# Kernel optimization log

Hardware: AMD Instinct MI355X
Metric: run time of the kernel (lower is better)

The kernel has to match this reference:

```python
import jax, jax.numpy as jnp
import numpy as np

N_NODES = 100000
N_EDGES = 1600000
IN_FEATS = 256
N_HEADS = 4
OUT_FEATS = 32
NEG_SLOPE = 0.2


def setup_inputs() -> dict:
    key = jax.random.key(0)
    k0, k1, k2, k3, k4, k5 = jax.random.split(key, 6)
    feat = jax.random.normal(k0, (N_NODES, IN_FEATS), dtype=jnp.float32)
    src = jax.random.randint(k1, (N_EDGES,), 0, N_NODES, dtype=jnp.int32)
    dst = jax.random.randint(k2, (N_EDGES,), 0, N_NODES, dtype=jnp.int32)
    # fc.weight: [num_heads*out_feats, in_feats] (torch Linear layout)
    W = jax.random.normal(k3, (N_HEADS * OUT_FEATS, IN_FEATS), dtype=jnp.float32) * 0.05
    attn_l = jax.random.normal(k4, (1, N_HEADS, OUT_FEATS), dtype=jnp.float32) * 0.1
    attn_r = jax.random.normal(k5, (1, N_HEADS, OUT_FEATS), dtype=jnp.float32) * 0.1
    return {"feat": feat, "src": src, "dst": dst, "W": W, "attn_l": attn_l, "attn_r": attn_r}


def reference(feat, src, dst, W, attn_l, attn_r):
    N = feat.shape[0]
    H, D = attn_l.shape[1], attn_l.shape[2]
    # fc projection -> [N, H, D]
    feat_src = (feat @ W.T).reshape(N, H, D)
    el = jnp.sum(feat_src * attn_l, axis=-1)  # [N, H]
    er = jnp.sum(feat_src * attn_r, axis=-1)  # [N, H]
    # per-edge scores: u_add_v then LeakyReLU  -> [E, H]
    e = jax.nn.leaky_relu(el[src] + er[dst], negative_slope=NEG_SLOPE)
    # edge_softmax: segmented softmax over edges grouped by destination node
    emax = jax.ops.segment_max(e, dst, num_segments=N)  # [N, H]
    emax = jnp.where(jnp.isfinite(emax), emax, jnp.zeros_like(emax))
    ee = jnp.exp(e - emax[dst])  # [E, H]
    denom = jax.ops.segment_sum(ee, dst, num_segments=N)  # [N, H]
    a = ee / denom[dst]  # [E, H]
    # u_mul_e + sum aggregation -> [N, H, D]
    m = feat_src[src] * a[:, :, None]  # [E, H, D]
    rst = jax.ops.segment_sum(m, dst, num_segments=N)
    return rst
```

## Files before the change

### kernel.cpp

```cpp
#include <hip/hip_runtime.h>
#include <hip/hip_bf16.h>
#include <math.h>

#define NN 100000
#define NE 1600000
#define INF_ 256
#define NH 4
#define DH 32
#define NHD 128
#define NEG_SLOPE 0.2f

#define NBC 391
#define STRIDEC 4608
#define EPBC 4096
#define NBLK_BIN 391
#define GEMM_BLKS 782
#define FMAX 1408
#define SMEM_BYTES 37504

typedef __attribute__((ext_vector_type(8))) short bf16x8;
typedef __attribute__((ext_vector_type(4))) float f32x4;

__device__ __forceinline__ unsigned short f2bf(float f) {
    __hip_bfloat16 b = __float2bfloat16(f);
    return *reinterpret_cast<unsigned short*>(&b);
}

__global__ __launch_bounds__(256) void k_prep0(const float* __restrict__ W,
                                               unsigned short* __restrict__ Wimg,
                                               int* __restrict__ gcur) {
    int t = threadIdx.x;
    int b = blockIdx.x;
    if (b == 16) {
        for (int i = t; i < NBC; i += 256) gcur[i] = 0;
        return;
    }
    int i = b * 256 + t;
    int kt = i >> 9;
    int r = (i >> 2) & 127;
    int g = i & 3;
    int slot = g ^ (r & 7);
    const float* s = &W[(size_t)r * INF_ + kt * 32 + g * 8];
    unsigned short tmp[8];
#pragma unroll
    for (int j = 0; j < 8; j++) tmp[j] = f2bf(s[j]);
    *(bf16x8*)&Wimg[(size_t)kt * 8192 + r * 64 + slot * 8] = *(const bf16x8*)tmp;
}

__global__ __launch_bounds__(256) void k_gemmbin(const float* __restrict__ feat,
                                                 const unsigned short* __restrict__ Wimg,
                                                 const int* __restrict__ src,
                                                 const int* __restrict__ dst,
                                                 const float* __restrict__ al,
                                                 const float* __restrict__ ar,
                                                 unsigned short* __restrict__ fsb,
                                                 float* __restrict__ el,
                                                 float* __restrict__ er,
                                                 int* __restrict__ gcur,
                                                 unsigned* __restrict__ packed) {
    __shared__ __align__(16) char smem[SMEM_BYTES];
    const int t = threadIdx.x;

    if (blockIdx.x >= GEMM_BLKS) {
        int hb = blockIdx.x - GEMM_BLKS;
        unsigned* lrec = (unsigned*)smem;
        int* lgpos = (int*)(smem + 16384);
        int* lc   = (int*)(smem + 32768);
        int* wb   = lc + NBC;
        int* loff = wb + NBC;
        int* wsum = loff + NBC;
        for (int i = t; i < NBC; i += 256) lc[i] = 0;
        __syncthreads();
        int base = hb * EPBC;
#pragma unroll 4
        for (int j = 0; j < 16; j++) {
            int e = base + j * 256 + t;
            if (e < NE) atomicAdd(&lc[dst[e] >> 8], 1);
        }
        __syncthreads();
        int i0 = t * 2;
        int c0 = (i0 < NBC) ? lc[i0] : 0;
        int c1 = (i0 + 1 < NBC) ? lc[i0 + 1] : 0;
        int s2 = c0 + c1;
        int lane = t & 63, w = t >> 6;
        int x = s2;
#pragma unroll
        for (int o = 1; o < 64; o <<= 1) {
            int y = __shfl_up(x, o);
            if (lane >= o) x += y;
        }
        if (lane == 63) wsum[w] = x;
        __syncthreads();
        int add = 0;
        for (int j = 0; j < w; j++) add += wsum[j];
        int ex = add + x - s2;
        if (i0 < NBC) loff[i0] = ex;
        if (i0 + 1 < NBC) loff[i0 + 1] = ex + c0;
        for (int i = t; i < NBC; i += 256) {
            int c = lc[i];
            wb[i] = c ? i * STRIDEC + atomicAdd(&gcur[i], c) : 0;
        }
        __syncthreads();
        for (int i = t; i < NBC; i += 256) lc[i] = loff[i];
        __syncthreads();
#pragma unroll 4
        for (int j = 0; j < 16; j++) {
            int e = base + j * 256 + t;
            if (e < NE) {
                int d = dst[e];
                int bk = d >> 8;
                int pos = atomicAdd(&lc[bk], 1);
                lrec[pos] = ((unsigned)src[e] << 8) | (unsigned)(d & 255);
                int g = wb[bk] + (pos - loff[bk]);
                lgpos[pos] = (g < (bk + 1) * STRIDEC) ? g : -1;
            }
        }
        __syncthreads();
        int nedge = NE - base;
        if (nedge > EPBC) nedge = EPBC;
        for (int i = t; i < nedge; i += 256) {
            int g = lgpos[i];
            if (g >= 0) packed[g] = lrec[i];
        }
        return;
    }

    short* sA = (short*)smem;
    short* sB = (short*)(smem + 16384);
    const int brow = blockIdx.x * 128;
    const int wid = t >> 6, lane = t & 63;
    const int wr = wid >> 1, wc = wid & 1;
    const int lg = lane >> 4;
    const int lr = lane & 15;

    f32x4 acc[4][4];
#pragma unroll
    for (int m = 0; m < 4; m++)
#pragma unroll
        for (int n = 0; n < 4; n++) acc[m][n] = (f32x4){0.f, 0.f, 0.f, 0.f};

    const int srow = t >> 1;
    const int cb = (t & 1) * 16;
    const int g0 = cb >> 3;
    const int p0 = (g0 ^ (srow & 7));
    const int p1 = ((g0 + 1) ^ (srow & 7));
    const int grow = brow + srow;
    const bool arow_ok = (grow < NN);
    const char* bimg = (const char*)Wimg;

    float fv[16];
    uint4 wv0, wv1, wv2, wv3;
    if (arow_ok) {
        const float4* pa = (const float4*)&feat[(size_t)grow * INF_ + cb];
        *(float4*)&fv[0] = pa[0];
        *(float4*)&fv[4] = pa[1];
        *(float4*)&fv[8] = pa[2];
        *(float4*)&fv[12] = pa[3];
    } else {
#pragma unroll
        for (int j = 0; j < 16; j++) fv[j] = 0.f;
    }
    wv0 = *(const uint4*)(bimg + t * 16);
    wv1 = *(const uint4*)(bimg + 4096 + t * 16);
    wv2 = *(const uint4*)(bimg + 8192 + t * 16);
    wv3 = *(const uint4*)(bimg + 12288 + t * 16);

    for (int kt = 0; kt < 8; kt++) {
        {
            short sv[16];
#pragma unroll
            for (int j = 0; j < 16; j++) sv[j] = (short)f2bf(fv[j]);
            *(bf16x8*)&sA[srow * 64 + p0 * 8] = *(const bf16x8*)&sv[0];
            *(bf16x8*)&sA[srow * 64 + p1 * 8] = *(const bf16x8*)&sv[8];
            char* bd = (char*)sB;
            *(uint4*)(bd + t * 16) = wv0;
            *(uint4*)(bd + 4096 + t * 16) = wv1;
            *(uint4*)(bd + 8192 + t * 16) = wv2;
            *(uint4*)(bd + 12288 + t * 16) = wv3;
        }
        __syncthreads();
        if (kt < 7) {
            int k0 = (kt + 1) * 32;
            if (arow_ok) {
                const float4* pa = (const float4*)&feat[(size_t)grow * INF_ + k0 + cb];
                *(float4*)&fv[0] = pa[0];
                *(float4*)&fv[4] = pa[1];
                *(float4*)&fv[8] = pa[2];
                *(float4*)&fv[12] = pa[3];
            }
            const char* bsrc = bimg + (size_t)(kt + 1) * 16384;
            wv0 = *(const uint4*)(bsrc + t * 16);
            wv1 = *(const uint4*)(bsrc + 4096 + t * 16);
            wv2 = *(const uint4*)(bsrc + 8192 + t * 16);
            wv3 = *(const uint4*)(bsrc + 12288 + t * 16);
        }
        bf16x8 aF[4], bF[4];
#pragma unroll
        for (int m = 0; m < 4; m++) {
            int r = wr * 64 + m * 16 + lr;
            aF[m] = *(const bf16x8*)&sA[r * 64 + ((lg ^ (r & 7)) * 8)];
        }
#pragma unroll
        for (int n = 0; n < 4; n++) {
            int r = wc * 64 + n * 16 + lr;
            bF[n] = *(const bf16x8*)&sB[r * 64 + ((lg ^ (r & 7)) * 8)];
        }
#pragma unroll
        for (int m = 0; m < 4; m++)
#pragma unroll
            for (int n = 0; n < 4; n++)
                acc[m][n] = __builtin_amdgcn_mfma_f32_16x16x32_bf16(aF[m], bF[n], acc[m][n], 0, 0, 0);
        __syncthreads();
    }
#pragma unroll
    for (int m = 0; m < 4; m++) {
#pragma unroll
        for (int n = 0; n < 4; n++) {
#pragma unroll
            for (int r = 0; r < 4; r++) {
                int gr = brow + wr * 64 + m * 16 + lg * 4 + r;
                if (gr < NN)
                    fsb[(size_t)gr * NHD + wc * 64 + n * 16 + lr] = f2bf(acc[m][n][r]);
            }
        }
    }
    const int hA = wc * 2, hB = wc * 2 + 1;
    const float alA0 = al[hA * 32 + lr], alA1 = al[hA * 32 + 16 + lr];
    const float alB0 = al[hB * 32 + lr], alB1 = al[hB * 32 + 16 + lr];
    const float arA0 = ar[hA * 32 + lr], arA1 = ar[hA * 32 + 16 + lr];
    const float arB0 = ar[hB * 32 + lr], arB1 = ar[hB * 32 + 16 + lr];
#pragma unroll
    for (int m = 0; m < 4; m++) {
#pragma unroll
        for (int r = 0; r < 4; r++) {
            float eA = acc[m][0][r] * alA0 + acc[m][1][r] * alA1;
            float eB = acc[m][2][r] * alB0 + acc[m][3][r] * alB1;
            float fA = acc[m][0][r] * arA0 + acc[m][1][r] * arA1;
            float fB = acc[m][2][r] * arB0 + acc[m][3][r] * arB1;
#pragma unroll
            for (int off = 1; off < 16; off <<= 1) {
                eA += __shfl_xor(eA, off);
                eB += __shfl_xor(eB, off);
                fA += __shfl_xor(fA, off);
                fB += __shfl_xor(fB, off);
            }
            if (lr == 0) {
                int gr = brow + wr * 64 + m * 16 + lg * 4 + r;
                if (gr < NN) {
                    el[gr * 4 + hA] = eA;
                    el[gr * 4 + hB] = eB;
                    er[gr * 4 + hA] = fA;
                    er[gr * 4 + hB] = fB;
                }
            }
        }
    }
}

__global__ __launch_bounds__(256) void k_sortagg(const int* __restrict__ gcur,
                                                 const unsigned* __restrict__ packed,
                                                 const float* __restrict__ el,
                                                 const float* __restrict__ er,
                                                 const uint4* __restrict__ fsb128,
                                                 float* __restrict__ out) {
    __shared__ int lh[64];
    __shared__ int off[65];
    __shared__ int cur[64];
    __shared__ int esrc_l[FMAX];
    int bq = blockIdx.x;
    int b = bq >> 2, quarter = bq & 3;
    int t = threadIdx.x;
    int beg = b * STRIDEC;
    int cnt = gcur[b];
    if (cnt > STRIDEC) cnt = STRIDEC;

    if (t < 64) lh[t] = 0;
    __syncthreads();
    for (int k = t; k < cnt; k += 256) {
        unsigned p = packed[beg + k];
        if (((p >> 6) & 3u) == (unsigned)quarter) atomicAdd(&lh[p & 63u], 1);
    }
    __syncthreads();
    if (t < 64) {
        int v = lh[t];
        int x = v;
#pragma unroll
        for (int o = 1; o < 64; o <<= 1) {
            int y = __shfl_up(x, o);
            if (t >= o) x += y;
        }
        off[t] = x - v;
        cur[t] = x - v;
        if (t == 63) off[64] = x;
    }
    __syncthreads();
    for (int k = t; k < cnt; k += 256) {
        unsigned p = packed[beg + k];
        if (((p >> 6) & 3u) == (unsigned)quarter) {
            int pos = atomicAdd(&cur[p & 63u], 1);
            if (pos < FMAX) esrc_l[pos] = (int)(p >> 8);
        }
    }
    __syncthreads();

    int lane = t & 63;
    int wv = t >> 6;
    int q = lane >> 4;
    int sl = lane & 15;
    int h = sl >> 2;

#define STEP(eV, vV)                                           \
    {                                                          \
        float sc_ = (eV) + rr;                                 \
        sc_ = sc_ > 0.f ? sc_ : NEG_SLOPE * sc_;               \
        float ee = __expf(sc_);                                \
        den += ee;                                             \
        a0 += ee * __uint_as_float((vV).x << 16);              \
        a1 += ee * __uint_as_float((vV).x & 0xFFFF0000u);      \
        a2 += ee * __uint_as_float((vV).y << 16);              \
        a3 += ee * __uint_as_float((vV).y & 0xFFFF0000u);      \
        a4 += ee * __uint_as_float((vV).z << 16);              \
        a5 += ee * __uint_as_float((vV).z & 0xFFFF0000u);      \
        a6 += ee * __uint_as_float((vV).w << 16);              \
        a7 += ee * __uint_as_float((vV).w & 0xFFFF0000u);      \
    }

    for (int ln = wv * 16; ln < wv * 16 + 16; ln++) {
        int node = (b << 8) + (quarter << 6) + ln;
        if (node >= NN) break;
        int bg = off[ln];
        int en = off[ln + 1];
        if (en > FMAX) en = FMAX;
        float rr = er[node * 4 + h];
        float den = 0.f;
        float a0 = 0.f, a1 = 0.f, a2 = 0.f, a3 = 0.f;
        float a4 = 0.f, a5 = 0.f, a6 = 0.f, a7 = 0.f;
        int k = bg + q;
        for (; k + 4 < en; k += 8) {
            int s0 = esrc_l[k];
            int s1 = esrc_l[k + 4];
            uint4 v0 = fsb128[(size_t)s0 * 16 + sl];
            uint4 v1 = fsb128[(size_t)s1 * 16 + sl];
            float e0 = el[s0 * 4 + h];
            float e1 = el[s1 * 4 + h];
            STEP(e0, v0)
            STEP(e1, v1)
        }
        for (; k < en; k += 4) {
            int s = esrc_l[k];
            uint4 vv = fsb128[(size_t)s * 16 + sl];
            float eV = el[s * 4 + h];
            STEP(eV, vv)
        }
#pragma unroll
        for (int o = 16; o <= 32; o <<= 1) {
            a0 += __shfl_xor(a0, o);
            a1 += __shfl_xor(a1, o);
            a2 += __shfl_xor(a2, o);
            a3 += __shfl_xor(a3, o);
            a4 += __shfl_xor(a4, o);
            a5 += __shfl_xor(a5, o);
            a6 += __shfl_xor(a6, o);
            a7 += __shfl_xor(a7, o);
            den += __shfl_xor(den, o);
        }
        if (q == 0) {
            float inv = den > 0.f ? 1.0f / den : 0.f;
            float4 o0, o1;
            o0.x = a0 * inv; o0.y = a1 * inv; o0.z = a2 * inv; o0.w = a3 * inv;
            o1.x = a4 * inv; o1.y = a5 * inv; o1.z = a6 * inv; o1.w = a7 * inv;
            float* p = &out[(size_t)node * NHD + sl * 8];
            *(float4*)p = o0;
            *(float4*)(p + 4) = o1;
        }
    }
#undef STEP
}

extern "C" void kernel_launch(void* const* d_in, const int* in_sizes, int n_in,
                              void* d_out, int out_size, void* d_ws, size_t ws_size,
                              hipStream_t stream) {
    const float* feat = (const float*)d_in[0];
    const int* src = (const int*)d_in[1];
    const int* dst = (const int*)d_in[2];
    const float* W = (const float*)d_in[3];
    const float* al = (const float*)d_in[4];
    const float* ar = (const float*)d_in[5];
    float* out = (float*)d_out;

    char* ws = (char*)d_ws;
    unsigned short* fsb = (unsigned short*)ws;   ws += (size_t)NN * NHD * 2;
    unsigned* packed = (unsigned*)ws;            ws += (size_t)NBC * STRIDEC * 4;
    float* el = (float*)ws;                      ws += (size_t)NN * NH * 4;
    float* er = (float*)ws;                      ws += (size_t)NN * NH * 4;
    int* gcur = (int*)ws;                        ws += (size_t)NBC * 4;
    unsigned short* Wimg = (unsigned short*)ws;  ws += (size_t)8 * 8192 * 2;

    k_prep0<<<17, 256, 0, stream>>>(W, Wimg, gcur);
    k_gemmbin<<<GEMM_BLKS + NBLK_BIN, 256, 0, stream>>>(feat, Wimg, src, dst,
                                                        al, ar, fsb, el, er,
                                                        gcur, packed);
    k_sortagg<<<NBC * 4, 256, 0, stream>>>(gcur, packed, el, er,
                                           (const uint4*)fsb, out);
}
```

Baseline: 146.2 us.

## Assign one destination node per 16-lane group and split buckets into eighths

The aggregation kernel now splits each 256-node bucket into eighths instead of quarters, launching twice as many blocks with a smaller shared edge list. Each 16-lane group handles a whole destination node on its own, so the cross-group shuffle reduction goes away and the edge loop is unrolled by four to keep more gathers in flight. The cost is that each block rescans the full bucket's packed edge list, doubling that redundant read traffic, and load balance now depends on per-node degree variance within a group.

```diff
diff --git a/kernel.cpp b/kernel.cpp
--- a/kernel.cpp
+++ b/kernel.cpp
@@ -15,7 +15,7 @@
 #define EPBC 4096
 #define NBLK_BIN 391
 #define GEMM_BLKS 782
-#define FMAX 1408
+#define FMAX 768
 #define SMEM_BYTES 37504
 
 typedef __attribute__((ext_vector_type(8))) short bf16x8;
@@ -263,41 +263,41 @@
                                                  const float* __restrict__ er,
                                                  const uint4* __restrict__ fsb128,
                                                  float* __restrict__ out) {
-    __shared__ int lh[64];
-    __shared__ int off[65];
-    __shared__ int cur[64];
+    __shared__ int lh[32];
+    __shared__ int off[33];
+    __shared__ int cur[32];
     __shared__ int esrc_l[FMAX];
     int bq = blockIdx.x;
-    int b = bq >> 2, quarter = bq & 3;
+    int b = bq >> 3, eighth = bq & 7;
     int t = threadIdx.x;
     int beg = b * STRIDEC;
     int cnt = gcur[b];
     if (cnt > STRIDEC) cnt = STRIDEC;
 
-    if (t < 64) lh[t] = 0;
+    if (t < 32) lh[t] = 0;
     __syncthreads();
     for (int k = t; k < cnt; k += 256) {
         unsigned p = packed[beg + k];
-        if (((p >> 6) & 3u) == (unsigned)quarter) atomicAdd(&lh[p & 63u], 1);
+        if (((p >> 5) & 7u) == (unsigned)eighth) atomicAdd(&lh[p & 31u], 1);
     }
     __syncthreads();
-    if (t < 64) {
+    if (t < 32) {
         int v = lh[t];
         int x = v;
 #pragma unroll
-        for (int o = 1; o < 64; o <<= 1) {
+        for (int o = 1; o < 32; o <<= 1) {
             int y = __shfl_up(x, o);
             if (t >= o) x += y;
         }
         off[t] = x - v;
         cur[t] = x - v;
-        if (t == 63) off[64] = x;
+        if (t == 31) off[32] = x;
     }
     __syncthreads();
     for (int k = t; k < cnt; k += 256) {
         unsigned p = packed[beg + k];
-        if (((p >> 6) & 3u) == (unsigned)quarter) {
-            int pos = atomicAdd(&cur[p & 63u], 1);
+        if (((p >> 5) & 7u) == (unsigned)eighth) {
+            int pos = atomicAdd(&cur[p & 31u], 1);
             if (pos < FMAX) esrc_l[pos] = (int)(p >> 8);
         }
     }
@@ -305,7 +305,7 @@
 
     int lane = t & 63;
     int wv = t >> 6;
-    int q = lane >> 4;
+    int g = lane >> 4;
     int sl = lane & 15;
     int h = sl >> 2;
 
@@ -325,46 +325,44 @@
         a7 += ee * __uint_as_float((vV).w & 0xFFFF0000u);      \
     }
 
-    for (int ln = wv * 16; ln < wv * 16 + 16; ln++) {
-        int node = (b << 8) + (quarter << 6) + ln;
-        if (node >= NN) break;
-        int bg = off[ln];
-        int en = off[ln + 1];
+#pragma unroll
+    for (int r = 0; r < 2; r++) {
+        int ln = wv * 8 + r * 4 + g;
+        int node = (b << 8) + (eighth << 5) + ln;
+        bool ok = (node < NN);
+        int bg = ok ? off[ln] : 0;
+        int en = ok ? off[ln + 1] : 0;
         if (en > FMAX) en = FMAX;
-        float rr = er[node * 4 + h];
+        float rr = ok ? er[node * 4 + h] : 0.f;
         float den = 0.f;
         float a0 = 0.f, a1 = 0.f, a2 = 0.f, a3 = 0.f;
         float a4 = 0.f, a5 = 0.f, a6 = 0.f, a7 = 0.f;
-        int k = bg + q;
-        for (; k + 4 < en; k += 8) {
+        int k = bg;
+        for (; k + 3 < en; k += 4) {
             int s0 = esrc_l[k];
-            int s1 = esrc_l[k + 4];
+            int s1 = esrc_l[k + 1];
+            int s2 = esrc_l[k + 2];
+            int s3 = esrc_l[k + 3];
             uint4 v0 = fsb128[(size_t)s0 * 16 + sl];
             uint4 v1 = fsb128[(size_t)s1 * 16 + sl];
+            uint4 v2 = fsb128[(size_t)s2 * 16 + sl];
+            uint4 v3 = fsb128[(size_t)s3 * 16 + sl];
             float e0 = el[s0 * 4 + h];
             float e1 = el[s1 * 4 + h];
+            float e2 = el[s2 * 4 + h];
+            float e3 = el[s3 * 4 + h];
             STEP(e0, v0)
             STEP(e1, v1)
-        }
-        for (; k < en; k += 4) {
+            STEP(e2, v2)
+            STEP(e3, v3)
+        }
+        for (; k < en; k++) {
             int s = esrc_l[k];
             uint4 vv = fsb128[(size_t)s * 16 + sl];
             float eV = el[s * 4 + h];
             STEP(eV, vv)
         }
-#pragma unroll
-        for (int o = 16; o <= 32; o <<= 1) {
-            a0 += __shfl_xor(a0, o);
-            a1 += __shfl_xor(a1, o);
-            a2 += __shfl_xor(a2, o);
-            a3 += __shfl_xor(a3, o);
-            a4 += __shfl_xor(a4, o);
-            a5 += __shfl_xor(a5, o);
-            a6 += __shfl_xor(a6, o);
-            a7 += __shfl_xor(a7, o);
-            den += __shfl_xor(den, o);
-        }
-        if (q == 0) {
+        if (ok) {
             float inv = den > 0.f ? 1.0f / den : 0.f;
             float4 o0, o1;
             o0.x = a0 * inv; o0.y = a1 * inv; o0.z = a2 * inv; o0.w = a3 * inv;
@@ -400,6 +398,6 @@
     k_gemmbin<<<GEMM_BLKS + NBLK_BIN, 256, 0, stream>>>(feat, Wimg, src, dst,
                                                         al, ar, fsb, el, er,
                                                         gcur, packed);
-    k_sortagg<<<NBC * 4, 256, 0, stream>>>(gcur, packed, el, er,
+    k_sortagg<<<NBC * 8, 256, 0, stream>>>(gcur, packed, el, er,
                                            (const uint4*)fsb, out);
 }
```

New measurement: 150.3 us. 2.8% more time.

## Split sort and aggregation into separate kernels with one wavefront per node

Applied to the files above, without the earlier changes.

The fused sort+aggregate kernel becomes two kernels. The first does a full per-bucket counting sort of packed edges into a global CSR-like esrc array plus per-node offset/count metadata. The second assigns one 64-lane wavefront per destination node. The binning blocks now come first in the grid and store a 16-bit bucket id instead of a precomputed global position, which shrinks shared memory. This targets load imbalance and the quadruple rescanning of packed edges, at the cost of an extra launch and an esrc global write and read.

```diff
diff --git a/kernel.cpp b/kernel.cpp
--- a/kernel.cpp
+++ b/kernel.cpp
@@ -15,8 +15,7 @@
 #define EPBC 4096
 #define NBLK_BIN 391
 #define GEMM_BLKS 782
-#define FMAX 1408
-#define SMEM_BYTES 37504
+#define SMEM_BYTES 32768
 
 typedef __attribute__((ext_vector_type(8))) short bf16x8;
 typedef __attribute__((ext_vector_type(4))) float f32x4;
@@ -61,11 +60,11 @@
     __shared__ __align__(16) char smem[SMEM_BYTES];
     const int t = threadIdx.x;
 
-    if (blockIdx.x >= GEMM_BLKS) {
-        int hb = blockIdx.x - GEMM_BLKS;
+    if (blockIdx.x < NBLK_BIN) {
+        int hb = blockIdx.x;
         unsigned* lrec = (unsigned*)smem;
-        int* lgpos = (int*)(smem + 16384);
-        int* lc   = (int*)(smem + 32768);
+        unsigned short* lbk = (unsigned short*)(smem + 16384);
+        int* lc   = (int*)(smem + 24576);
         int* wb   = lc + NBC;
         int* loff = wb + NBC;
         int* wsum = loff + NBC;
@@ -111,23 +110,24 @@
                 int bk = d >> 8;
                 int pos = atomicAdd(&lc[bk], 1);
                 lrec[pos] = ((unsigned)src[e] << 8) | (unsigned)(d & 255);
-                int g = wb[bk] + (pos - loff[bk]);
-                lgpos[pos] = (g < (bk + 1) * STRIDEC) ? g : -1;
+                lbk[pos] = (unsigned short)bk;
             }
         }
         __syncthreads();
         int nedge = NE - base;
         if (nedge > EPBC) nedge = EPBC;
         for (int i = t; i < nedge; i += 256) {
-            int g = lgpos[i];
-            if (g >= 0) packed[g] = lrec[i];
+            int bk = lbk[i];
+            int g = wb[bk] + (i - loff[bk]);
+            if (g < (bk + 1) * STRIDEC)
+                packed[g] = lrec[i];
         }
         return;
     }
 
     short* sA = (short*)smem;
     short* sB = (short*)(smem + 16384);
-    const int brow = blockIdx.x * 128;
+    const int brow = (blockIdx.x - NBLK_BIN) * 128;
     const int wid = t >> 6, lane = t & 63;
     const int wr = wid >> 1, wc = wid & 1;
     const int lg = lane >> 4;
@@ -257,57 +257,72 @@
     }
 }
 
-__global__ __launch_bounds__(256) void k_sortagg(const int* __restrict__ gcur,
-                                                 const unsigned* __restrict__ packed,
-                                                 const float* __restrict__ el,
-                                                 const float* __restrict__ er,
-                                                 const uint4* __restrict__ fsb128,
-                                                 float* __restrict__ out) {
-    __shared__ int lh[64];
-    __shared__ int off[65];
-    __shared__ int cur[64];
-    __shared__ int esrc_l[FMAX];
-    int bq = blockIdx.x;
-    int b = bq >> 2, quarter = bq & 3;
-    int t = threadIdx.x;
+__global__ __launch_bounds__(256) void k_sort(const int* __restrict__ gcur,
+                                              const unsigned* __restrict__ packed,
+                                              int* __restrict__ esrc,
+                                              int2* __restrict__ rowmeta) {
+    __shared__ int lh[256];
+    __shared__ int off[256];
+    __shared__ int cur[256];
+    __shared__ int wsum[4];
+    __shared__ int es[STRIDEC];
+    int b = blockIdx.x, t = threadIdx.x;
     int beg = b * STRIDEC;
     int cnt = gcur[b];
     if (cnt > STRIDEC) cnt = STRIDEC;
 
-    if (t < 64) lh[t] = 0;
+    lh[t] = 0;
+    __syncthreads();
+    for (int k = t; k < cnt; k += 256)
+        atomicAdd(&lh[packed[beg + k] & 255u], 1);
+    __syncthreads();
+    int v = lh[t];
+    int lane = t & 63, w = t >> 6;
+    int x = v;
+#pragma unroll
+    for (int o = 1; o < 64; o <<= 1) {
+        int y = __shfl_up(x, o);
+        if (lane >= o) x += y;
+    }
+    if (lane == 63) wsum[w] = x;
+    __syncthreads();
+    int add = 0;
+    for (int j = 0; j < w; j++) add += wsum[j];
+    int excl = add + x - v;
+    off[t] = excl;
+    cur[t] = excl;
+    int node = (b << 8) + t;
+    if (node < NN) rowmeta[node] = make_int2(beg + excl, v);
     __syncthreads();
     for (int k = t; k < cnt; k += 256) {
         unsigned p = packed[beg + k];
-        if (((p >> 6) & 3u) == (unsigned)quarter) atomicAdd(&lh[p & 63u], 1);
+        int pos = atomicAdd(&cur[p & 255u], 1);
+        es[pos] = (int)(p >> 8);
     }
     __syncthreads();
-    if (t < 64) {
-        int v = lh[t];
-        int x = v;
-#pragma unroll
-        for (int o = 1; o < 64; o <<= 1) {
-            int y = __shfl_up(x, o);
-            if (t >= o) x += y;
-        }
-        off[t] = x - v;
-        cur[t] = x - v;
-        if (t == 63) off[64] = x;
-    }
-    __syncthreads();
-    for (int k = t; k < cnt; k += 256) {
-        unsigned p = packed[beg + k];
-        if (((p >> 6) & 3u) == (unsigned)quarter) {
-            int pos = atomicAdd(&cur[p & 63u], 1);
-            if (pos < FMAX) esrc_l[pos] = (int)(p >> 8);
-        }
-    }
-    __syncthreads();
-
-    int lane = t & 63;
-    int wv = t >> 6;
+    for (int k = t; k < cnt; k += 256) esrc[beg + k] = es[k];
+}
+
+__global__ __launch_bounds__(256) void k_agg(const int2* __restrict__ rowmeta,
+                                             const int* __restrict__ esrc,
+                                             const float* __restrict__ el,
+                                             const float* __restrict__ er,
+                                             const uint4* __restrict__ fsb128,
+                                             float* __restrict__ out) {
+    int gid = blockIdx.x * blockDim.x + threadIdx.x;
+    int node = gid >> 6;
+    int lane = gid & 63;
+    if (node >= NN) return;
     int q = lane >> 4;
     int sl = lane & 15;
     int h = sl >> 2;
+    int2 md = rowmeta[node];
+    int beg = md.x;
+    int end = md.x + md.y;
+    float rr = er[node * 4 + h];
+    float den = 0.f;
+    float a0 = 0.f, a1 = 0.f, a2 = 0.f, a3 = 0.f;
+    float a4 = 0.f, a5 = 0.f, a6 = 0.f, a7 = 0.f;
 
 #define STEP(eV, vV)                                           \
     {                                                          \
@@ -325,56 +340,47 @@
         a7 += ee * __uint_as_float((vV).w & 0xFFFF0000u);      \
     }
 
-    for (int ln = wv * 16; ln < wv * 16 + 16; ln++) {
-        int node = (b << 8) + (quarter << 6) + ln;
-        if (node >= NN) break;
-        int bg = off[ln];
-        int en = off[ln + 1];
-        if (en > FMAX) en = FMAX;
-        float rr = er[node * 4 + h];
-        float den = 0.f;
-        float a0 = 0.f, a1 = 0.f, a2 = 0.f, a3 = 0.f;
-        float a4 = 0.f, a5 = 0.f, a6 = 0.f, a7 = 0.f;
-        int k = bg + q;
-        for (; k + 4 < en; k += 8) {
-            int s0 = esrc_l[k];
-            int s1 = esrc_l[k + 4];
-            uint4 v0 = fsb128[(size_t)s0 * 16 + sl];
-            uint4 v1 = fsb128[(size_t)s1 * 16 + sl];
-            float e0 = el[s0 * 4 + h];
-            float e1 = el[s1 * 4 + h];
-            STEP(e0, v0)
-            STEP(e1, v1)
-        }
-        for (; k < en; k += 4) {
-            int s = esrc_l[k];
-            uint4 vv = fsb128[(size_t)s * 16 + sl];
-            float eV = el[s * 4 + h];
-            STEP(eV, vv)
-        }
-#pragma unroll
-        for (int o = 16; o <= 32; o <<= 1) {
-            a0 += __shfl_xor(a0, o);
-            a1 += __shfl_xor(a1, o);
-            a2 += __shfl_xor(a2, o);
-            a3 += __shfl_xor(a3, o);
-            a4 += __shfl_xor(a4, o);
-            a5 += __shfl_xor(a5, o);
-            a6 += __shfl_xor(a6, o);
-            a7 += __shfl_xor(a7, o);
-            den += __shfl_xor(den, o);
-        }
-        if (q == 0) {
-            float inv = den > 0.f ? 1.0f / den : 0.f;
-            float4 o0, o1;
-            o0.x = a0 * inv; o0.y = a1 * inv; o0.z = a2 * inv; o0.w = a3 * inv;
-            o1.x = a4 * inv; o1.y = a5 * inv; o1.z = a6 * inv; o1.w = a7 * inv;
-            float* p = &out[(size_t)node * NHD + sl * 8];
-            *(float4*)p = o0;
-            *(float4*)(p + 4) = o1;
-        }
+    int k = beg + q;
+    for (; k + 4 < end; k += 8) {
+        int s0 = esrc[k];
+        int s1 = esrc[k + 4];
+        uint4 v0 = fsb128[(size_t)s0 * 16 + sl];
+        uint4 v1 = fsb128[(size_t)s1 * 16 + sl];
+        float e0 = el[s0 * 4 + h];
+        float e1 = el[s1 * 4 + h];
+        STEP(e0, v0)
+        STEP(e1, v1)
+    }
+    for (; k < end; k += 4) {
+        int s = esrc[k];
+        uint4 v = fsb128[(size_t)s * 16 + sl];
+        float eV = el[s * 4 + h];
+        STEP(eV, v)
     }
 #undef STEP
+
+#pragma unroll
+    for (int o = 16; o <= 32; o <<= 1) {
+        a0 += __shfl_xor(a0, o);
+        a1 += __shfl_xor(a1, o);
+        a2 += __shfl_xor(a2, o);
+        a3 += __shfl_xor(a3, o);
+        a4 += __shfl_xor(a4, o);
+        a5 += __shfl_xor(a5, o);
+        a6 += __shfl_xor(a6, o);
+        a7 += __shfl_xor(a7, o);
+        den += __shfl_xor(den, o);
+    }
+
+    if (q == 0) {
+        float inv = den > 0.f ? 1.0f / den : 0.f;
+        float4 o0, o1;
+        o0.x = a0 * inv; o0.y = a1 * inv; o0.z = a2 * inv; o0.w = a3 * inv;
+        o1.x = a4 * inv; o1.y = a5 * inv; o1.z = a6 * inv; o1.w = a7 * inv;
+        float* p = &out[(size_t)node * NHD + sl * 8];
+        *(float4*)p = o0;
+        *(float4*)(p + 4) = o1;
+    }
 }
 
 extern "C" void kernel_launch(void* const* d_in, const int* in_sizes, int n_in,
@@ -391,8 +397,10 @@
     char* ws = (char*)d_ws;
     unsigned short* fsb = (unsigned short*)ws;   ws += (size_t)NN * NHD * 2;
     unsigned* packed = (unsigned*)ws;            ws += (size_t)NBC * STRIDEC * 4;
+    int* esrc = (int*)ws;                        ws += (size_t)NBC * STRIDEC * 4;
     float* el = (float*)ws;                      ws += (size_t)NN * NH * 4;
     float* er = (float*)ws;                      ws += (size_t)NN * NH * 4;
+    int2* rowmeta = (int2*)ws;                   ws += (size_t)NN * 8;
     int* gcur = (int*)ws;                        ws += (size_t)NBC * 4;
     unsigned short* Wimg = (unsigned short*)ws;  ws += (size_t)8 * 8192 * 2;
 
@@ -400,6 +408,7 @@
     k_gemmbin<<<GEMM_BLKS + NBLK_BIN, 256, 0, stream>>>(feat, Wimg, src, dst,
                                                         al, ar, fsb, el, er,
                                                         gcur, packed);
-    k_sortagg<<<NBC * 4, 256, 0, stream>>>(gcur, packed, el, er,
-                                           (const uint4*)fsb, out);
-}
+    k_sort<<<NBC, 256, 0, stream>>>(gcur, packed, esrc, rowmeta);
+    k_agg<<<(NN * 64 + 255) / 256, 256, 0, stream>>>(rowmeta, esrc, el, er,
+                                                     (const uint4*)fsb, out);
+}
```

Result: faster. 141.1 us (-3.5%).
